# Kernel tuning notes

Hardware: AMD Instinct MI355X
Metric: run time of the kernel (lower is better)

Reference implementation:

```python
import jax, jax.numpy as jnp
import numpy as np

HIDDEN = 2048
HEADS = 16
HEAD_DIM = HIDDEN // HEADS  # 128
B, S = 2, 2048


def setup_inputs() -> dict:
    key = jax.random.key(0)
    ks = jax.random.split(key, 9)
    s_in = 1.0 / np.sqrt(HIDDEN)
    return {
        "X": jax.random.normal(ks[0], (B, S, HIDDEN), dtype=jnp.float32),
        "attention_mask": jnp.ones((B, S, S), dtype=jnp.int32),
        "Wq": jax.random.uniform(ks[1], (HIDDEN, HIDDEN), jnp.float32, -s_in, s_in),
        "bq": jax.random.uniform(ks[2], (HIDDEN,), jnp.float32, -s_in, s_in),
        "Wk": jax.random.uniform(ks[3], (HIDDEN, HEAD_DIM), jnp.float32, -s_in, s_in),
        "bk": jax.random.uniform(ks[4], (HEAD_DIM,), jnp.float32, -s_in, s_in),
        "Wv": jax.random.uniform(ks[5], (HIDDEN, HEAD_DIM), jnp.float32, -s_in, s_in),
        "bv": jax.random.uniform(ks[6], (HEAD_DIM,), jnp.float32, -s_in, s_in),
        "Wo": jax.random.uniform(ks[7], (HIDDEN, HIDDEN), jnp.float32, -s_in, s_in),
        "bo": jax.random.uniform(ks[8], (HIDDEN,), jnp.float32, -s_in, s_in),
    }


def reference(X, attention_mask, Wq, bq, Wk, bk, Wv, bv, Wo, bo):
    b, s, _ = X.shape
    # Projections
    Q = X @ Wq + bq                      # (B, S, H*D)
    K = X @ Wk + bk                      # (B, S, D)  shared across heads (MQA)
    V = X @ Wv + bv                      # (B, S, D)
    Q = Q.reshape(b, s, HEADS, HEAD_DIM).transpose(0, 2, 1, 3)  # (B, H, S, D)
    scale = 1.0 / jnp.sqrt(jnp.float32(HEAD_DIM))
    # QK^T with shared K head
    scores = jnp.einsum('bhqd,bkd->bhqk', Q, K) * scale          # (B, H, S, S)
    scores = jnp.where(attention_mask[:, None, :, :] == 0, -jnp.inf, scores)
    attn = jax.nn.softmax(scores, axis=-1)
    # dropout_rate = 0.0 (eval) -> identity
    out = jnp.einsum('bhqk,bkd->bhqd', attn, V)                  # (B, H, S, D)
    out = out.transpose(0, 2, 1, 3).reshape(b, s, HIDDEN)        # (B, S, hidden)
    return out @ Wo + bo
```

## Files before the change

kernel.cpp:

```cpp
#include <hip/hip_runtime.h>
#include <cstdint>
#include <cstddef>

#define HIDDEN 2048
#define HEADS 16
#define HD 128
#define BSZ 2
#define SEQ 2048
#define MTOT (BSZ * SEQ)
#define NQKV (HIDDEN + 2 * HD)
#define SL2E 0.12751743f

typedef unsigned short ushort_t;
typedef __attribute__((ext_vector_type(8))) __bf16 bf16x8;
typedef __attribute__((ext_vector_type(4))) float f32x4;
typedef __attribute__((ext_vector_type(16))) float f32x16;

typedef __attribute__((address_space(3))) unsigned int as3_u32;
typedef __attribute__((address_space(1))) const unsigned int as1_u32;

__device__ __forceinline__ ushort_t f2bf(float x) {
  union { float f; unsigned u; } v; v.f = x;
  unsigned r = v.u + 0x7fffu + ((v.u >> 16) & 1u);
  return (ushort_t)(r >> 16);
}
__device__ __forceinline__ unsigned pk_bf16(float a, float b) {
  union { float f; unsigned u; } x, y; x.f = a; y.f = b;
  return (x.u >> 16) | (y.u & 0xFFFF0000u);
}

__device__ __forceinline__ void gld16(const void* g, void* lds) {
  __builtin_amdgcn_global_load_lds((as1_u32*)g, (as3_u32*)lds, 16, 0, 0);
}

__global__ __launch_bounds__(256) void cvt_bf16_kernel(
    const float* __restrict__ in, ushort_t* __restrict__ out, int n4) {
  int i = blockIdx.x * 256 + threadIdx.x;
  if (i >= n4) return;
  float4 v = ((const float4*)in)[i];
  ushort4 o;
  o.x = f2bf(v.x); o.y = f2bf(v.y); o.z = f2bf(v.z); o.w = f2bf(v.w);
  ((ushort4*)out)[i] = o;
}

__global__ __launch_bounds__(256) void cvtT_qkv_kernel(
    const float* __restrict__ Wq, const float* __restrict__ Wk,
    const float* __restrict__ Wv, ushort_t* __restrict__ WT) {
  __shared__ float tile[32][36];
  const int t = threadIdx.x;
  const int nb = blockIdx.x * 32, kb = blockIdx.y * 32;
  const float* W; int N, nc; float scale;
  if (nb < HIDDEN)            { W = Wq; N = HIDDEN; nc = nb;               scale = SL2E; }
  else if (nb < HIDDEN + HD)  { W = Wk; N = HD;     nc = nb - HIDDEN;      scale = 1.f; }
  else                        { W = Wv; N = HD;     nc = nb - HIDDEN - HD; scale = 1.f; }
  {
    int row = t >> 3, c4 = (t & 7) << 2;
    float4 v = *(const float4*)(W + (size_t)(kb + row) * N + nc + c4);
    tile[row][c4] = v.x * scale; tile[row][c4 + 1] = v.y * scale;
    tile[row][c4 + 2] = v.z * scale; tile[row][c4 + 3] = v.w * scale;
  }
  __syncthreads();
  {
    int nl = t >> 3, k4 = (t & 7) << 2;
    ushort4 o;
    o.x = f2bf(tile[k4 + 0][nl]); o.y = f2bf(tile[k4 + 1][nl]);
    o.z = f2bf(tile[k4 + 2][nl]); o.w = f2bf(tile[k4 + 3][nl]);
    *(ushort4*)(WT + (size_t)(nb + nl) * HIDDEN + kb + k4) = o;
  }
}

__global__ __launch_bounds__(256) void cvtT_kernel(
    const float* __restrict__ W, ushort_t* __restrict__ WT, int K, int N) {
  __shared__ float tile[32][36];
  const int t = threadIdx.x;
  const int kb = blockIdx.y * 32, nb = blockIdx.x * 32;
  {
    int row = t >> 3, c4 = (t & 7) << 2;
    float4 v = *(const float4*)(W + (size_t)(kb + row) * N + nb + c4);
    tile[row][c4] = v.x; tile[row][c4 + 1] = v.y;
    tile[row][c4 + 2] = v.z; tile[row][c4 + 3] = v.w;
  }
  __syncthreads();
  {
    int nl = t >> 3, k4 = (t & 7) << 2;
    ushort4 o;
    o.x = f2bf(tile[k4 + 0][nl]); o.y = f2bf(tile[k4 + 1][nl]);
    o.z = f2bf(tile[k4 + 2][nl]); o.w = f2bf(tile[k4 + 3][nl]);
    *(ushort4*)(WT + (size_t)(nb + nl) * K + kb + k4) = o;
  }
}

__global__ __launch_bounds__(256) void transpose_v_kernel(
    const ushort_t* __restrict__ Vin, ushort_t* __restrict__ Vt) {
  __shared__ ushort_t tile[32][40];
  const int t = threadIdx.x;
  const int rb = blockIdx.x * 32, cb = blockIdx.y * 32;
  {
    int row = t >> 3, c4 = (t & 7) << 2;
    ushort4 v = *(const ushort4*)(Vin + (size_t)(rb + row) * NQKV + cb + c4);
    tile[row][c4] = v.x; tile[row][c4 + 1] = v.y;
    tile[row][c4 + 2] = v.z; tile[row][c4 + 3] = v.w;
  }
  __syncthreads();
  {
    int dl = t >> 3, r4 = (t & 7) << 2;
    ushort4 o;
    o.x = tile[r4 + 0][dl]; o.y = tile[r4 + 1][dl];
    o.z = tile[r4 + 2][dl]; o.w = tile[r4 + 3][dl];
    *(ushort4*)(Vt + (size_t)(cb + dl) * MTOT + rb + r4) = o;
  }
}

__global__ void concat_bias_kernel(const float* __restrict__ bq,
                                   const float* __restrict__ bk,
                                   const float* __restrict__ bv,
                                   float* __restrict__ o) {
  int i = blockIdx.x * 256 + threadIdx.x;
  if (i >= NQKV) return;
  o[i] = (i < HIDDEN) ? bq[i] * SL2E
       : (i < HIDDEN + HD ? bk[i - HIDDEN] : bv[i - HIDDEN - HD]);
}

__global__ __launch_bounds__(256) void mask_flags_kernel(
    const int* __restrict__ mask, int* __restrict__ flags) {
  const int kt = blockIdx.x, qt = blockIdx.y, b = blockIdx.z;
  const int t = threadIdx.x;
  int allv = 1, anyv = 0;
  const size_t base = (size_t)b * SEQ * SEQ + (size_t)qt * 128 * SEQ + kt * 64;
  for (int i = t; i < 2048; i += 256) {
    const int row = i >> 4, c4 = (i & 15) << 2;
    const int4 v = *(const int4*)(mask + base + (size_t)row * SEQ + c4);
    const int nz = (v.x != 0) & (v.y != 0) & (v.z != 0) & (v.w != 0);
    const int nzany = (v.x != 0) | (v.y != 0) | (v.z != 0) | (v.w != 0);
    allv &= nz; anyv |= nzany;
  }
  const int wAll = __all(allv), wAny = __any(anyv);
  __shared__ int sA[4], sO[4];
  if ((t & 63) == 0) { sA[t >> 6] = wAll; sO[t >> 6] = wAny; }
  __syncthreads();
  if (t == 0) {
    const int A = sA[0] & sA[1] & sA[2] & sA[3];
    const int O = sO[0] | sO[1] | sO[2] | sO[3];
    flags[(b * 16 + qt) * 32 + kt] = A ? 2 : (O ? 1 : 0);
  }
}

template <int OUTF32>
__global__ __launch_bounds__(256) void gemm_mfma(
    const ushort_t* __restrict__ A, const ushort_t* __restrict__ Bt,
    const float* __restrict__ bias, void* __restrict__ C,
    int M, int N, int K, int nm_per_xcd) {
  __shared__ ushort_t As[2][128 * 64];
  __shared__ ushort_t Bs[2][128 * 64];
  const int t = threadIdx.x;
  const int w = t >> 6, l = t & 63;
  const int id = blockIdx.x;
  const int xcd = id & 7, j = id >> 3;
  const int mt = xcd * nm_per_xcd + (j % nm_per_xcd);
  const int nt = j / nm_per_xcd;
  const int mb = mt * 128, nb = nt * 128;
  const int wm = (w >> 1) * 64, wn = (w & 1) * 64;
  const int fl = l & 15, g = l >> 4;
  const int srow = l >> 3, cphys = l & 7;

  f32x4 acc[4][4];
#pragma unroll
  for (int i = 0; i < 4; ++i)
#pragma unroll
    for (int jj = 0; jj < 4; ++jj) acc[i][jj] = (f32x4){0.f, 0.f, 0.f, 0.f};

#pragma unroll
  for (int jj = 0; jj < 4; ++jj) {
    const int inst = w * 4 + jj;
    const int row = inst * 8 + srow;
    const int clog = cphys ^ (row & 7);
    gld16(A + (size_t)(mb + row) * K + clog * 8, &As[0][inst * 512]);
    gld16(Bt + (size_t)(nb + row) * K + clog * 8, &Bs[0][inst * 512]);
  }

  int cur = 0;
  for (int k0 = 0; k0 < K; k0 += 64) {
    __syncthreads();
    if (k0 + 64 < K) {
#pragma unroll
      for (int jj = 0; jj < 4; ++jj) {
        const int inst = w * 4 + jj;
        const int row = inst * 8 + srow;
        const int clog = cphys ^ (row & 7);
        gld16(A + (size_t)(mb + row) * K + k0 + 64 + clog * 8,
              &As[cur ^ 1][inst * 512]);
        gld16(Bt + (size_t)(nb + row) * K + k0 + 64 + clog * 8,
              &Bs[cur ^ 1][inst * 512]);
      }
    }
    const ushort_t* Ac = &As[cur][0];
    const ushort_t* Bc = &Bs[cur][0];
#pragma unroll
    for (int s = 0; s < 2; ++s) {
      bf16x8 af[4], bfr[4];
#pragma unroll
      for (int i = 0; i < 4; ++i) {
        const int m = wm + i * 16 + fl;
        af[i] = *(const bf16x8*)&Ac[m * 64 + (((s << 2) + g) ^ (m & 7)) * 8];
        const int n = wn + i * 16 + fl;
        bfr[i] = *(const bf16x8*)&Bc[n * 64 + (((s << 2) + g) ^ (n & 7)) * 8];
      }
#pragma unroll
      for (int i = 0; i < 4; ++i)
#pragma unroll
        for (int jj = 0; jj < 4; ++jj)
          acc[i][jj] = __builtin_amdgcn_mfma_f32_16x16x32_bf16(
              af[i], bfr[jj], acc[i][jj], 0, 0, 0);
    }
    cur ^= 1;
  }

#pragma unroll
  for (int jj = 0; jj < 4; ++jj) {
    const int col = nb + wn + jj * 16 + fl;
    const float bv = bias[col];
#pragma unroll
    for (int i = 0; i < 4; ++i) {
      const int row0 = mb + wm + i * 16 + g * 4;
#pragma unroll
      for (int r = 0; r < 4; ++r) {
        const float val = acc[i][jj][r] + bv;
        if (OUTF32)
          ((float*)C)[(size_t)(row0 + r) * N + col] = val;
        else
          ((ushort_t*)C)[(size_t)(row0 + r) * N + col] = f2bf(val);
      }
    }
  }
}

__global__ __launch_bounds__(256, 2) void flash_mfma(
    const ushort_t* __restrict__ QKV,
    const ushort_t* __restrict__ Vt,
    const int* __restrict__ mask,
    const int* __restrict__ flags,
    ushort_t* __restrict__ Ab)
{
  __shared__ ushort_t Kbuf[2][64 * 128];
  __shared__ ushort_t Vbuf[2][128 * 64];

  const int qt = blockIdx.x, h = blockIdx.y, b = blockIdx.z;
  const int t = threadIdx.x, w = t >> 6, l = t & 63;
  const int q31 = l & 31, hi = l >> 5;
  const int qbase = qt * 128;
  const int qrow = qbase + w * 32 + q31;

  bf16x8 qf[8];
#pragma unroll
  for (int ks = 0; ks < 8; ++ks)
    qf[ks] = *(const bf16x8*)(QKV + (size_t)(b * SEQ + qrow) * NQKV + h * HD +
                              ks * 16 + hi * 8);

  bf16x8 onesf;
  {
    const ushort_t ov = (q31 == 0) ? (ushort_t)0x3F80 : (ushort_t)0;
#pragma unroll
    for (int jj = 0; jj < 8; ++jj) ((ushort_t*)&onesf)[jj] = ov;
  }

#pragma unroll
  for (int j = 0; j < 4; ++j) {
    const int inst = w * 4 + j;
    const int krow = inst * 4 + (l >> 4);
    const int ck = (l & 15) ^ (krow & 15);
    gld16(QKV + (size_t)(b * SEQ + krow) * NQKV + HIDDEN + ck * 8,
          &Kbuf[0][inst * 512]);
    const int drow = inst * 8 + (l >> 3);
    const int cv = (l & 7) ^ (drow & 7);
    gld16(Vt + (size_t)drow * MTOT + b * SEQ + cv * 8, &Vbuf[0][inst * 512]);
  }

  const size_t mbase = (size_t)b * SEQ * SEQ;

  f32x16 oacc[4], lacc;
#pragma unroll
  for (int d = 0; d < 4; ++d)
#pragma unroll
    for (int r = 0; r < 16; ++r) oacc[d][r] = 0.f;
#pragma unroll
  for (int r = 0; r < 16; ++r) lacc[r] = 0.f;

  int cur = 0;
  for (int kt = 0; kt < SEQ / 64; ++kt) {
    const int kbase = kt * 64;
    const int flag = flags[((b * 16 + qt) << 5) + kt];
    __syncthreads();

    {
      const int knb = (kt + 1 < SEQ / 64) ? (kbase + 64) : kbase;
#pragma unroll
      for (int j = 0; j < 4; ++j) {
        const int inst = w * 4 + j;
        const int krow = inst * 4 + (l >> 4);
        const int ck = (l & 15) ^ (krow & 15);
        gld16(QKV + (size_t)(b * SEQ + knb + krow) * NQKV + HIDDEN + ck * 8,
              &Kbuf[cur ^ 1][inst * 512]);
        const int drow = inst * 8 + (l >> 3);
        const int cv = (l & 7) ^ (drow & 7);
        gld16(Vt + (size_t)drow * MTOT + b * SEQ + knb + cv * 8,
              &Vbuf[cur ^ 1][inst * 512]);
      }
    }

    const ushort_t* Kc = &Kbuf[cur][0];
    f32x16 sc[2];
#pragma unroll
    for (int kk = 0; kk < 2; ++kk)
#pragma unroll
      for (int r = 0; r < 16; ++r) sc[kk][r] = 0.f;

    __builtin_amdgcn_s_setprio(1);
#pragma unroll
    for (int ks = 0; ks < 8; ++ks)
#pragma unroll
      for (int kk = 0; kk < 2; ++kk) {
        const int key = kk * 32 + q31;
        const bf16x8 kf = *(const bf16x8*)&Kc[key * 128 +
                                              (((ks << 1) + hi) ^ (key & 15)) * 8];
        sc[kk] = __builtin_amdgcn_mfma_f32_32x32x16_bf16(kf, qf[ks], sc[kk],
                                                         0, 0, 0);
      }
    __builtin_amdgcn_s_setprio(0);

    if (flag != 2) {
#pragma unroll
      for (int kk = 0; kk < 2; ++kk)
#pragma unroll
        for (int r = 0; r < 16; ++r) {
          const int key = kbase + kk * 32 + (r & 3) + ((r >> 2) << 3) + (hi << 2);
          if (!mask[mbase + (size_t)qrow * SEQ + key]) sc[kk][r] = -1e30f;
        }
    }

    bf16x8 pa[4];
#pragma unroll
    for (int kk = 0; kk < 2; ++kk) {
      float pv[16];
#pragma unroll
      for (int r = 0; r < 16; ++r) pv[r] = __builtin_amdgcn_exp2f(sc[kk][r]);
#pragma unroll
      for (int half = 0; half < 2; ++half) {
        const int bs = half * 8;
        unsigned a0 = pk_bf16(pv[bs + 0], pv[bs + 1]);
        unsigned a1 = pk_bf16(pv[bs + 2], pv[bs + 3]);
        unsigned b0 = pk_bf16(pv[bs + 4], pv[bs + 5]);
        unsigned b1 = pk_bf16(pv[bs + 6], pv[bs + 7]);
        asm("v_permlane32_swap_b32 %0, %1" : "+v"(a0), "+v"(b0));
        asm("v_permlane32_swap_b32 %0, %1" : "+v"(a1), "+v"(b1));
        union { unsigned u[4]; bf16x8 v; } uu;
        uu.u[0] = a0; uu.u[1] = a1; uu.u[2] = b0; uu.u[3] = b1;
        pa[kk * 2 + half] = uu.v;
      }
    }

    const ushort_t* Vc = &Vbuf[cur][0];
    __builtin_amdgcn_s_setprio(1);
#pragma unroll
    for (int ks = 0; ks < 4; ++ks) {
#pragma unroll
      for (int dt = 0; dt < 4; ++dt) {
        const int d = dt * 32 + q31;
        const bf16x8 vf = *(const bf16x8*)&Vc[d * 64 +
                                              (((ks << 1) + hi) ^ (d & 7)) * 8];
        oacc[dt] = __builtin_amdgcn_mfma_f32_32x32x16_bf16(pa[ks], vf,
                                                           oacc[dt], 0, 0, 0);
      }
      lacc = __builtin_amdgcn_mfma_f32_32x32x16_bf16(pa[ks], onesf, lacc,
                                                     0, 0, 0);
    }
    __builtin_amdgcn_s_setprio(0);
    cur ^= 1;
  }

#pragma unroll
  for (int r = 0; r < 16; ++r) {
    const float ls = __shfl(lacc[r], l & 32, 64);
    const float invl = 1.0f / ls;
    const int row = b * SEQ + qbase + w * 32 + (r & 3) + ((r >> 2) << 3) +
                    (hi << 2);
#pragma unroll
    for (int dt = 0; dt < 4; ++dt)
      Ab[(size_t)row * HIDDEN + h * HD + dt * 32 + q31] =
          f2bf(oacc[dt][r] * invl);
  }
}

extern "C" void kernel_launch(void* const* d_in, const int* in_sizes, int n_in,
                              void* d_out, int out_size, void* d_ws, size_t ws_size,
                              hipStream_t stream) {
  const float* X  = (const float*)d_in[0];
  const int* mask = (const int*)d_in[1];
  const float* Wq = (const float*)d_in[2];
  const float* bq = (const float*)d_in[3];
  const float* Wk = (const float*)d_in[4];
  const float* bk = (const float*)d_in[5];
  const float* Wv = (const float*)d_in[6];
  const float* bv = (const float*)d_in[7];
  const float* Wo = (const float*)d_in[8];
  const float* bo = (const float*)d_in[9];
  float* out = (float*)d_out;

  char* p = (char*)d_ws;
  ushort_t* QKVb = (ushort_t*)p; p += (size_t)MTOT * NQKV * 2;
  ushort_t* Xb   = (ushort_t*)p; p += (size_t)MTOT * HIDDEN * 2;
  ushort_t* WT   = (ushort_t*)p; p += (size_t)NQKV * HIDDEN * 2;
  ushort_t* WoT  = (ushort_t*)p; p += (size_t)HIDDEN * HIDDEN * 2;
  ushort_t* Vt   = (ushort_t*)p; p += (size_t)HD * MTOT * 2;
  float* biasQKV = (float*)p;    p += 4096;
  int* flags     = (int*)p;      p += BSZ * 16 * 32 * 4;
  ushort_t* Ab = Xb;

  cvt_bf16_kernel<<<(MTOT * HIDDEN / 4 + 255) / 256, 256, 0, stream>>>(
      X, Xb, MTOT * HIDDEN / 4);
  cvtT_qkv_kernel<<<dim3(NQKV / 32, HIDDEN / 32), 256, 0, stream>>>(
      Wq, Wk, Wv, WT);
  cvtT_kernel<<<dim3(HIDDEN / 32, HIDDEN / 32), 256, 0, stream>>>(
      Wo, WoT, HIDDEN, HIDDEN);
  concat_bias_kernel<<<(NQKV + 255) / 256, 256, 0, stream>>>(bq, bk, bv, biasQKV);
  mask_flags_kernel<<<dim3(32, 16, BSZ), 256, 0, stream>>>(mask, flags);

  gemm_mfma<0><<<dim3((MTOT / 128) * (NQKV / 128)), 256, 0, stream>>>(
      Xb, WT, biasQKV, QKVb, MTOT, NQKV, HIDDEN, (MTOT / 128) / 8);
  transpose_v_kernel<<<dim3(MTOT / 32, HD / 32), 256, 0, stream>>>(
      QKVb + HIDDEN + HD, Vt);
  flash_mfma<<<dim3(SEQ / 128, HEADS, BSZ), 256, 0, stream>>>(
      QKVb, Vt, mask, flags, Ab);
  gemm_mfma<1><<<dim3((MTOT / 128) * (HIDDEN / 128)), 256, 0, stream>>>(
      Ab, WoT, bo, out, MTOT, HIDDEN, HIDDEN, (MTOT / 128) / 8);
}
```

Baseline: 340.2 us.

## Give each flash-attention wave two query tiles and compute row sums on VALU

```diff
diff --git a/kernel.cpp b/kernel.cpp
--- a/kernel.cpp
+++ b/kernel.cpp
@@ -27,6 +27,11 @@
 __device__ __forceinline__ unsigned pk_bf16(float a, float b) {
   union { float f; unsigned u; } x, y; x.f = a; y.f = b;
   return (x.u >> 16) | (y.u & 0xFFFF0000u);
+}
+__device__ __forceinline__ float truncbf(float x) {
+  union { float f; unsigned u; } v; v.f = x;
+  v.u &= 0xFFFF0000u;
+  return v.f;
 }
 
 __device__ __forceinline__ void gld16(const void* g, void* lds) {
@@ -234,7 +239,7 @@
   }
 }
 
-__global__ __launch_bounds__(256, 2) void flash_mfma(
+__global__ __launch_bounds__(128, 1) void flash_mfma(
     const ushort_t* __restrict__ QKV,
     const ushort_t* __restrict__ Vt,
     const int* __restrict__ mask,
@@ -242,48 +247,47 @@
     ushort_t* __restrict__ Ab)
 {
   __shared__ ushort_t Kbuf[2][64 * 128];
-  __shared__ ushort_t Vbuf[2][128 * 64];
+  __shared__ ushort_t Vbuf[2][64 * 128];
 
   const int qt = blockIdx.x, h = blockIdx.y, b = blockIdx.z;
   const int t = threadIdx.x, w = t >> 6, l = t & 63;
   const int q31 = l & 31, hi = l >> 5;
-  const int qbase = qt * 128;
-  const int qrow = qbase + w * 32 + q31;
-
-  bf16x8 qf[8];
-#pragma unroll
-  for (int ks = 0; ks < 8; ++ks)
-    qf[ks] = *(const bf16x8*)(QKV + (size_t)(b * SEQ + qrow) * NQKV + h * HD +
-                              ks * 16 + hi * 8);
-
-  bf16x8 onesf;
-  {
-    const ushort_t ov = (q31 == 0) ? (ushort_t)0x3F80 : (ushort_t)0;
-#pragma unroll
-    for (int jj = 0; jj < 8; ++jj) ((ushort_t*)&onesf)[jj] = ov;
-  }
-
-#pragma unroll
-  for (int j = 0; j < 4; ++j) {
-    const int inst = w * 4 + j;
+  const int qbase = qt * 128 + w * 64;
+
+  bf16x8 qf[2][8];
+#pragma unroll
+  for (int qs = 0; qs < 2; ++qs) {
+    const int qrow = qbase + qs * 32 + q31;
+#pragma unroll
+    for (int ks = 0; ks < 8; ++ks)
+      qf[qs][ks] = *(const bf16x8*)(QKV + (size_t)(b * SEQ + qrow) * NQKV +
+                                    h * HD + ks * 16 + hi * 8);
+  }
+
+#pragma unroll
+  for (int j = 0; j < 8; ++j) {
+    const int inst = w * 8 + j;
     const int krow = inst * 4 + (l >> 4);
     const int ck = (l & 15) ^ (krow & 15);
     gld16(QKV + (size_t)(b * SEQ + krow) * NQKV + HIDDEN + ck * 8,
           &Kbuf[0][inst * 512]);
-    const int drow = inst * 8 + (l >> 3);
-    const int cv = (l & 7) ^ (drow & 7);
-    gld16(Vt + (size_t)drow * MTOT + b * SEQ + cv * 8, &Vbuf[0][inst * 512]);
+    const int r = inst * 4 + (l >> 4);
+    const int clog = (l & 15) ^ (r & 15);
+    const int d = 2 * r + (clog >> 3);
+    gld16(Vt + (size_t)d * MTOT + b * SEQ + (clog & 7) * 8,
+          &Vbuf[0][inst * 512]);
   }
 
   const size_t mbase = (size_t)b * SEQ * SEQ;
 
-  f32x16 oacc[4], lacc;
-#pragma unroll
-  for (int d = 0; d < 4; ++d)
-#pragma unroll
-    for (int r = 0; r < 16; ++r) oacc[d][r] = 0.f;
-#pragma unroll
-  for (int r = 0; r < 16; ++r) lacc[r] = 0.f;
+  f32x16 oacc[2][4];
+#pragma unroll
+  for (int qs = 0; qs < 2; ++qs)
+#pragma unroll
+    for (int d = 0; d < 4; ++d)
+#pragma unroll
+      for (int r = 0; r < 16; ++r) oacc[qs][d][r] = 0.f;
+  float lsum[2] = {0.f, 0.f};
 
   int cur = 0;
   for (int kt = 0; kt < SEQ / 64; ++kt) {
@@ -294,25 +298,28 @@
     {
       const int knb = (kt + 1 < SEQ / 64) ? (kbase + 64) : kbase;
 #pragma unroll
-      for (int j = 0; j < 4; ++j) {
-        const int inst = w * 4 + j;
+      for (int j = 0; j < 8; ++j) {
+        const int inst = w * 8 + j;
         const int krow = inst * 4 + (l >> 4);
         const int ck = (l & 15) ^ (krow & 15);
         gld16(QKV + (size_t)(b * SEQ + knb + krow) * NQKV + HIDDEN + ck * 8,
               &Kbuf[cur ^ 1][inst * 512]);
-        const int drow = inst * 8 + (l >> 3);
-        const int cv = (l & 7) ^ (drow & 7);
-        gld16(Vt + (size_t)drow * MTOT + b * SEQ + knb + cv * 8,
+        const int r = inst * 4 + (l >> 4);
+        const int clog = (l & 15) ^ (r & 15);
+        const int d = 2 * r + (clog >> 3);
+        gld16(Vt + (size_t)d * MTOT + b * SEQ + knb + (clog & 7) * 8,
               &Vbuf[cur ^ 1][inst * 512]);
       }
     }
 
     const ushort_t* Kc = &Kbuf[cur][0];
-    f32x16 sc[2];
-#pragma unroll
-    for (int kk = 0; kk < 2; ++kk)
-#pragma unroll
-      for (int r = 0; r < 16; ++r) sc[kk][r] = 0.f;
+    f32x16 sc[2][2];
+#pragma unroll
+    for (int qs = 0; qs < 2; ++qs)
+#pragma unroll
+      for (int kk = 0; kk < 2; ++kk)
+#pragma unroll
+        for (int r = 0; r < 16; ++r) sc[qs][kk][r] = 0.f;
 
     __builtin_amdgcn_s_setprio(1);
 #pragma unroll
@@ -321,72 +328,95 @@
       for (int kk = 0; kk < 2; ++kk) {
         const int key = kk * 32 + q31;
         const bf16x8 kf = *(const bf16x8*)&Kc[key * 128 +
-                                              (((ks << 1) + hi) ^ (key & 15)) * 8];
-        sc[kk] = __builtin_amdgcn_mfma_f32_32x32x16_bf16(kf, qf[ks], sc[kk],
-                                                         0, 0, 0);
+                                              (((ks << 1) + hi) ^ (q31 & 15)) * 8];
+        sc[0][kk] = __builtin_amdgcn_mfma_f32_32x32x16_bf16(kf, qf[0][ks],
+                                                            sc[0][kk], 0, 0, 0);
+        sc[1][kk] = __builtin_amdgcn_mfma_f32_32x32x16_bf16(kf, qf[1][ks],
+                                                            sc[1][kk], 0, 0, 0);
       }
     __builtin_amdgcn_s_setprio(0);
 
     if (flag != 2) {
 #pragma unroll
-      for (int kk = 0; kk < 2; ++kk)
+      for (int qs = 0; qs < 2; ++qs) {
+        const int qrow = qbase + qs * 32 + q31;
+#pragma unroll
+        for (int kk = 0; kk < 2; ++kk)
+#pragma unroll
+          for (int r = 0; r < 16; ++r) {
+            const int key =
+                kbase + kk * 32 + (r & 3) + ((r >> 2) << 3) + (hi << 2);
+            if (!mask[mbase + (size_t)qrow * SEQ + key]) sc[qs][kk][r] = -1e30f;
+          }
+      }
+    }
+
+    bf16x8 pa[2][4];
+#pragma unroll
+    for (int qs = 0; qs < 2; ++qs) {
+#pragma unroll
+      for (int kk = 0; kk < 2; ++kk) {
+        float pv[16];
 #pragma unroll
         for (int r = 0; r < 16; ++r) {
-          const int key = kbase + kk * 32 + (r & 3) + ((r >> 2) << 3) + (hi << 2);
-          if (!mask[mbase + (size_t)qrow * SEQ + key]) sc[kk][r] = -1e30f;
+          pv[r] = __builtin_amdgcn_exp2f(sc[qs][kk][r]);
+          lsum[qs] += truncbf(pv[r]);
         }
-    }
-
-    bf16x8 pa[4];
-#pragma unroll
-    for (int kk = 0; kk < 2; ++kk) {
-      float pv[16];
-#pragma unroll
-      for (int r = 0; r < 16; ++r) pv[r] = __builtin_amdgcn_exp2f(sc[kk][r]);
-#pragma unroll
-      for (int half = 0; half < 2; ++half) {
-        const int bs = half * 8;
-        unsigned a0 = pk_bf16(pv[bs + 0], pv[bs + 1]);
-        unsigned a1 = pk_bf16(pv[bs + 2], pv[bs + 3]);
-        unsigned b0 = pk_bf16(pv[bs + 4], pv[bs + 5]);
-        unsigned b1 = pk_bf16(pv[bs + 6], pv[bs + 7]);
-        asm("v_permlane32_swap_b32 %0, %1" : "+v"(a0), "+v"(b0));
-        asm("v_permlane32_swap_b32 %0, %1" : "+v"(a1), "+v"(b1));
-        union { unsigned u[4]; bf16x8 v; } uu;
-        uu.u[0] = a0; uu.u[1] = a1; uu.u[2] = b0; uu.u[3] = b1;
-        pa[kk * 2 + half] = uu.v;
+#pragma unroll
+        for (int half = 0; half < 2; ++half) {
+          const int bs = half * 8;
+          unsigned a0 = pk_bf16(pv[bs + 0], pv[bs + 1]);
+          unsigned a1 = pk_bf16(pv[bs + 2], pv[bs + 3]);
+          unsigned b0 = pk_bf16(pv[bs + 4], pv[bs + 5]);
+          unsigned b1 = pk_bf16(pv[bs + 6], pv[bs + 7]);
+          asm("v_permlane32_swap_b32 %0, %1" : "+v"(a0), "+v"(b0));
+          asm("v_permlane32_swap_b32 %0, %1" : "+v"(a1), "+v"(b1));
+          union { unsigned u[4]; bf16x8 v; } uu;
+          uu.u[0] = a0; uu.u[1] = a1; uu.u[2] = b0; uu.u[3] = b1;
+          pa[qs][kk * 2 + half] = uu.v;
+        }
       }
     }
 
     const ushort_t* Vc = &Vbuf[cur][0];
     __builtin_amdgcn_s_setprio(1);
 #pragma unroll
-    for (int ks = 0; ks < 4; ++ks) {
+    for (int ks = 0; ks < 4; ++ks)
 #pragma unroll
       for (int dt = 0; dt < 4; ++dt) {
         const int d = dt * 32 + q31;
-        const bf16x8 vf = *(const bf16x8*)&Vc[d * 64 +
-                                              (((ks << 1) + hi) ^ (d & 7)) * 8];
-        oacc[dt] = __builtin_amdgcn_mfma_f32_32x32x16_bf16(pa[ks], vf,
-                                                           oacc[dt], 0, 0, 0);
-      }
-      lacc = __builtin_amdgcn_mfma_f32_32x32x16_bf16(pa[ks], onesf, lacc,
-                                                     0, 0, 0);
-    }
+        const int r = d >> 1;
+        const int clog = ((d & 1) << 3) + (ks << 1) + hi;
+        const bf16x8 vf =
+            *(const bf16x8*)&Vc[r * 128 + (clog ^ (r & 15)) * 8];
+        oacc[0][dt] = __builtin_amdgcn_mfma_f32_32x32x16_bf16(pa[0][ks], vf,
+                                                              oacc[0][dt], 0, 0, 0);
+        oacc[1][dt] = __builtin_amdgcn_mfma_f32_32x32x16_bf16(pa[1][ks], vf,
+                                                              oacc[1][dt], 0, 0, 0);
+      }
     __builtin_amdgcn_s_setprio(0);
     cur ^= 1;
   }
 
 #pragma unroll
-  for (int r = 0; r < 16; ++r) {
-    const float ls = __shfl(lacc[r], l & 32, 64);
-    const float invl = 1.0f / ls;
-    const int row = b * SEQ + qbase + w * 32 + (r & 3) + ((r >> 2) << 3) +
-                    (hi << 2);
-#pragma unroll
-    for (int dt = 0; dt < 4; ++dt)
-      Ab[(size_t)row * HIDDEN + h * HD + dt * 32 + q31] =
-          f2bf(oacc[dt][r] * invl);
+  for (int qs = 0; qs < 2; ++qs) {
+    unsigned a, bsw;
+    union { float f; unsigned u; } cv; cv.f = lsum[qs];
+    a = cv.u; bsw = cv.u;
+    asm("v_permlane32_swap_b32 %0, %1" : "+v"(a), "+v"(bsw));
+    union { unsigned u; float f; } fa, fb; fa.u = a; fb.u = bsw;
+    const float ltot = fa.f + fb.f;
+#pragma unroll
+    for (int r = 0; r < 16; ++r) {
+      const int crow = (r & 3) + ((r >> 2) << 3) + (hi << 2);
+      const float lv = __shfl(ltot, crow, 64);
+      const float invl = 1.0f / lv;
+      const int row = b * SEQ + qbase + qs * 32 + crow;
+#pragma unroll
+      for (int dt = 0; dt < 4; ++dt)
+        Ab[(size_t)row * HIDDEN + h * HD + dt * 32 + q31] =
+            f2bf(oacc[qs][dt][r] * invl);
+    }
   }
 }
 
@@ -428,7 +458,7 @@
       Xb, WT, biasQKV, QKVb, MTOT, NQKV, HIDDEN, (MTOT / 128) / 8);
   transpose_v_kernel<<<dim3(MTOT / 32, HD / 32), 256, 0, stream>>>(
       QKVb + HIDDEN + HD, Vt);
-  flash_mfma<<<dim3(SEQ / 128, HEADS, BSZ), 256, 0, stream>>>(
+  flash_mfma<<<dim3(SEQ / 128, HEADS, BSZ), 128, 0, stream>>>(
       QKVb, Vt, mask, flags, Ab);
   gemm_mfma<1><<<dim3((MTOT / 128) * (HIDDEN / 128)), 256, 0, stream>>>(
       Ab, WoT, bo, out, MTOT, HIDDEN, HIDDEN, (MTOT / 128) / 8);
```

After: 368.1 us. +8.2%, slower.
